# Optimization experiments

Measured on AMD Instinct MI355X. Metric: run time of the kernel, lower is better.

## Reference

```python
import jax, jax.numpy as jnp
import numpy as np

# Fixed hyperparameters matching init_kwargs
DIL_START = 2
DIL_END = 1024   # n_dilations = 1022
N_BULGE = 2
BATCH, L, C = 8, 2048, 4


def _variant_tables():
    """Static (forward_shift, backward_shift, has_GU) table, one row per output feature.
    Order per distance s: [main AU_CG+GU, left bulge d=1..n, right bulge d=1..n]."""
    f, b, g = [], [], []
    for s in range(DIL_START, DIL_END):
        f.append(s + 1); b.append(s + 1); g.append(1.0)            # dilate
        for d in range(1, N_BULGE + 1):                            # left bulge
            f.append(s + 1); b.append(s + 1 + d); g.append(0.0)
        for d in range(1, N_BULGE + 1):                            # right bulge
            f.append(s + 1 + d); b.append(s + 1); g.append(0.0)
    return np.array(f), np.array(b), np.array(g, dtype=np.float32)


def setup_inputs() -> dict:
    key = jax.random.key(0)
    x = jax.random.uniform(key, (BATCH, L, C), dtype=jnp.float32)
    return {"x": x}


def reference(x) -> jnp.ndarray:
    n, L_, _ = x.shape
    f_np, b_np, g_np = _variant_tables()
    f_arr = jnp.asarray(f_np)
    b_arr = jnp.asarray(b_np)
    gu_arr = jnp.asarray(g_np).astype(x.dtype)
    max_f = int(f_np.max())
    max_b = int(b_np.max())

    # y[i] = x[i+f] (zeros past the end);  z[i] = x[i-b] (zeros before start)
    xp_r = jnp.pad(x, ((0, 0), (0, max_f), (0, 0)))
    xp_l = jnp.pad(x, ((0, 0), (max_b, 0), (0, 0)))
    w4 = jnp.array([2.0, 3.0, 3.0, 2.0], dtype=x.dtype)  # AU/CG pairing weights

    def variant(f, b, g):
        y = jax.lax.dynamic_slice_in_dim(xp_r, f, L_, axis=1)          # (n, L, 4)
        z = jax.lax.dynamic_slice_in_dim(xp_l, max_b - b, L_, axis=1)  # (n, L, 4)
        # base: sum_c w[c] * x[i+f, c] * x[i-b, 3-c]  (reverse-complement correlation)
        base = jnp.einsum('nlc,nlc->nl', y * w4, z[..., ::-1])
        # GU wobble pairs (channels 2,3), weight 2, only for the non-bulge variant
        gu = 2.0 * (y[..., 2] * z[..., 3] + y[..., 3] * z[..., 2])
        return base + g * gu

    out = jax.vmap(variant)(f_arr, b_arr, gu_arr)  # (F, n, L)
    return jnp.transpose(out, (1, 2, 0))           # (n, L, F)
```

## Files before the change

### kernel.cpp

```cpp
#include <hip/hip_runtime.h>

#define LSEQ 2048
#define NS   1022
#define NF   5110
#define NB   8
#define IT   64
#define GI   4
#define NGRP (IT / GI)
#define TPB  256
#define FPB  (TPB * 5)

__device__ __forceinline__ float basescore(const float4 y, const float4 z) {
    return 2.f * y.x * z.w + 3.f * y.y * z.z + 3.f * y.z * z.y + 2.f * y.w * z.x;
}

__device__ __forceinline__ float4 loadx(const float4* __restrict__ xg, int p) {
    int pc = p < 0 ? 0 : (p > LSEQ - 1 ? LSEQ - 1 : p);
    float4 v = xg[pc];
    if ((unsigned)p >= (unsigned)LSEQ) v = make_float4(0.f, 0.f, 0.f, 0.f);
    return v;
}

__global__ __launch_bounds__(TPB) void fdcnn_kernel(const float4* __restrict__ x,
                                                    float* __restrict__ out) {
    __shared__ float st[2][GI][FPB];

    const int t = threadIdx.x;
    const int n = blockIdx.z;
    const float4* xg = x + (size_t)n * LSEQ;

    const int sidx = blockIdx.x * TPB + t;
    const int s = sidx + 2;
    const int i0 = blockIdx.y * IT;
    const int fbase = blockIdx.x * FPB;

    float4 yA = loadx(xg, i0 + s + 1);
    float4 yB = loadx(xg, i0 + s + 2);
    float4 zA = loadx(xg, i0 - s - 3);
    float4 zB = loadx(xg, i0 - s - 2);

    auto compute_group = [&](int g) {
        float* stg = &st[g & 1][0][0];
        #pragma unroll
        for (int ig = 0; ig < GI; ++ig) {
            const int i = i0 + g * GI + ig;
            float4 yC = loadx(xg, i + s + 3);
            float4 zC = loadx(xg, i - s - 1);
            const float4 y1 = yA, y2 = yB, y3 = yC;
            const float4 z3 = zA, z2 = zB, z1 = zC;
            float* sp = stg + ig * FPB + t * 5;
            sp[0] = basescore(y1, z1) + 2.f * (y1.z * z1.w + y1.w * z1.z);
            sp[1] = basescore(y1, z2);
            sp[2] = basescore(y1, z3);
            sp[3] = basescore(y2, z1);
            sp[4] = basescore(y3, z1);
            yA = yB; yB = yC;
            zA = zB; zB = zC;
        }
    };

    compute_group(0);

    for (int g = 0; g < NGRP; ++g) {
        asm volatile("s_waitcnt lgkmcnt(0)\n\ts_barrier" ::: "memory");

        if (g + 1 < NGRP) compute_group(g + 1);

        const float* stg = &st[g & 1][0][0];
        float* obase = out + ((size_t)n * LSEQ + (i0 + g * GI)) * (size_t)NF + fbase;
        #pragma unroll
        for (int k = 0; k < 5; ++k) {
            const int v  = k * TPB + t;
            const int ig = v / 320;
            const int fo = (v - ig * 320) * 4;
            const int rem = NF - (fbase + fo);
            const float4 val = *(const float4*)(stg + ig * FPB + fo);
            float* dst = obase + (size_t)ig * NF + fo;
            if (rem >= 4) {
                *(float4*)dst = val;
            } else if (rem > 0) {
                dst[0] = val.x;
                if (rem > 1) dst[1] = val.y;
            }
        }
    }
}

extern "C" void kernel_launch(void* const* d_in, const int* in_sizes, int n_in,
                              void* d_out, int out_size, void* d_ws, size_t ws_size,
                              hipStream_t stream) {
    const float4* x = (const float4*)d_in[0];
    float* out = (float*)d_out;
    dim3 grid((NS + TPB - 1) / TPB, LSEQ / IT, NB);
    dim3 block(TPB);
    fdcnn_kernel<<<grid, block, 0, stream>>>(x, out);
}
```

Baseline: 76.83 us.

## Interleave row groups across blocks and prefetch next group's inputs before stores

Each block now handles strided groups of 4 rows (stride 128 rows) instead of a contiguous 64-row tile, so concurrently running blocks write to rows spread across the output. The next group's inputs are loaded into registers before the current group's stores are issued, and the compute into shared memory happens after the stores, letting global loads overlap the write phase. Each group now reloads 6 float4 per sequence instead of sliding the window, and launch bounds ask for 4 blocks per CU. The output is a large store-bound tensor, so the gain depends on write locality and overlap.

```diff
diff --git a/kernel.cpp b/kernel.cpp
--- a/kernel.cpp
+++ b/kernel.cpp
@@ -4,9 +4,8 @@
 #define NS   1022
 #define NF   5110
 #define NB   8
-#define IT   64
 #define GI   4
-#define NGRP (IT / GI)
+#define NGRP 16
 #define TPB  256
 #define FPB  (TPB * 5)
 
@@ -21,53 +20,59 @@
     return v;
 }
 
-__global__ __launch_bounds__(TPB) void fdcnn_kernel(const float4* __restrict__ x,
-                                                    float* __restrict__ out) {
+__global__ __launch_bounds__(TPB, 4) void fdcnn_kernel(const float4* __restrict__ x,
+                                                       float* __restrict__ out) {
     __shared__ float st[2][GI][FPB];
 
     const int t = threadIdx.x;
+    const int bx = blockIdx.x;
+    const int by = blockIdx.y;
     const int n = blockIdx.z;
     const float4* xg = x + (size_t)n * LSEQ;
+    const int s = bx * TPB + t + 2;
+    const int fbase = bx * FPB;
 
-    const int sidx = blockIdx.x * TPB + t;
-    const int s = sidx + 2;
-    const int i0 = blockIdx.y * IT;
-    const int fbase = blockIdx.x * FPB;
-
-    float4 yA = loadx(xg, i0 + s + 1);
-    float4 yB = loadx(xg, i0 + s + 2);
-    float4 zA = loadx(xg, i0 - s - 3);
-    float4 zB = loadx(xg, i0 - s - 2);
-
-    auto compute_group = [&](int g) {
-        float* stg = &st[g & 1][0][0];
+    auto compute_to = [&](const float4* Y, const float4* Z, float* stg) {
         #pragma unroll
-        for (int ig = 0; ig < GI; ++ig) {
-            const int i = i0 + g * GI + ig;
-            float4 yC = loadx(xg, i + s + 3);
-            float4 zC = loadx(xg, i - s - 1);
-            const float4 y1 = yA, y2 = yB, y3 = yC;
-            const float4 z3 = zA, z2 = zB, z1 = zC;
-            float* sp = stg + ig * FPB + t * 5;
+        for (int ii = 0; ii < GI; ++ii) {
+            const float4 y1 = Y[ii], y2 = Y[ii + 1], y3 = Y[ii + 2];
+            const float4 z1 = Z[ii + 2], z2 = Z[ii + 1], z3 = Z[ii];
+            float* sp = stg + ii * FPB + t * 5;
             sp[0] = basescore(y1, z1) + 2.f * (y1.z * z1.w + y1.w * z1.z);
             sp[1] = basescore(y1, z2);
             sp[2] = basescore(y1, z3);
             sp[3] = basescore(y2, z1);
             sp[4] = basescore(y3, z1);
-            yA = yB; yB = yC;
-            zA = zB; zB = zC;
         }
     };
 
-    compute_group(0);
+    {
+        const int i0 = 4 * by;
+        float4 Y[6], Z[6];
+        #pragma unroll
+        for (int j = 0; j < 6; ++j) {
+            Y[j] = loadx(xg, i0 + s + 1 + j);
+            Z[j] = loadx(xg, i0 - s - 3 + j);
+        }
+        compute_to(Y, Z, &st[0][0][0]);
+    }
 
     for (int g = 0; g < NGRP; ++g) {
         asm volatile("s_waitcnt lgkmcnt(0)\n\ts_barrier" ::: "memory");
 
-        if (g + 1 < NGRP) compute_group(g + 1);
+        float4 Yn[6], Zn[6];
+        if (g + 1 < NGRP) {
+            const int i1 = 4 * (by + 32 * (g + 1));
+            #pragma unroll
+            for (int j = 0; j < 6; ++j) {
+                Yn[j] = loadx(xg, i1 + s + 1 + j);
+                Zn[j] = loadx(xg, i1 - s - 3 + j);
+            }
+        }
 
         const float* stg = &st[g & 1][0][0];
-        float* obase = out + ((size_t)n * LSEQ + (i0 + g * GI)) * (size_t)NF + fbase;
+        const int ig0 = 4 * (by + 32 * g);
+        float* obase = out + ((size_t)n * LSEQ + ig0) * (size_t)NF + fbase;
         #pragma unroll
         for (int k = 0; k < 5; ++k) {
             const int v  = k * TPB + t;
@@ -83,6 +88,8 @@
                 if (rem > 1) dst[1] = val.y;
             }
         }
+
+        if (g + 1 < NGRP) compute_to(Yn, Zn, &st[(g + 1) & 1][0][0]);
     }
 }
 
@@ -91,7 +98,7 @@
                               hipStream_t stream) {
     const float4* x = (const float4*)d_in[0];
     float* out = (float*)d_out;
-    dim3 grid((NS + TPB - 1) / TPB, LSEQ / IT, NB);
+    dim3 grid(4, 32, NB);
     dim3 block(TPB);
     fdcnn_kernel<<<grid, block, 0, stream>>>(x, out);
 }
```

New measurement: 73.43 us. -4.4%, faster.

## Stage input windows in per-wave LDS and drop block-wide barriers

Applied to the files above, without the earlier changes.

Each wave now loads its own sliding windows of x into shared memory once, instead of doing clamped global loads per row. The output staging buffer is also made per-wave, so the block-level s_barrier and the double buffering are removed. Each wave computes and stores its own strip of 320 features. The kernel is dominated by output writes, so the gain probably depends on whether removing barrier stalls lets stores stream more smoothly. The change also uses more LDS per block and sets a launch-bounds occupancy hint.

```diff
diff --git a/kernel.cpp b/kernel.cpp
--- a/kernel.cpp
+++ b/kernel.cpp
@@ -8,7 +8,9 @@
 #define GI   4
 #define NGRP (IT / GI)
 #define TPB  256
-#define FPB  (TPB * 5)
+#define NWAVE 4
+#define WSTRIP 320
+#define WLEN 132
 
 __device__ __forceinline__ float basescore(const float4 y, const float4 z) {
     return 2.f * y.x * z.w + 3.f * y.y * z.z + 3.f * y.z * z.y + 2.f * y.w * z.x;
@@ -21,34 +23,46 @@
     return v;
 }
 
-__global__ __launch_bounds__(TPB) void fdcnn_kernel(const float4* __restrict__ x,
-                                                    float* __restrict__ out) {
-    __shared__ float st[2][GI][FPB];
+__global__ __launch_bounds__(TPB, 4) void fdcnn_kernel(const float4* __restrict__ x,
+                                                       float* __restrict__ out) {
+    __shared__ float4 ysw[NWAVE][WLEN];
+    __shared__ float4 zsw[NWAVE][WLEN];
+    __shared__ float  stg[NWAVE][GI * WSTRIP];
 
     const int t = threadIdx.x;
+    const int w = t >> 6;
+    const int l = t & 63;
+    const int bx = blockIdx.x;
+    const int by = blockIdx.y;
     const int n = blockIdx.z;
+    const int i0 = by * IT;
     const float4* xg = x + (size_t)n * LSEQ;
 
-    const int sidx = blockIdx.x * TPB + t;
-    const int s = sidx + 2;
-    const int i0 = blockIdx.y * IT;
-    const int fbase = blockIdx.x * FPB;
+    const int s0 = bx * TPB + w * 64 + 2;
+    const int fwave = (bx * NWAVE + w) * WSTRIP;
 
-    float4 yA = loadx(xg, i0 + s + 1);
-    float4 yB = loadx(xg, i0 + s + 2);
-    float4 zA = loadx(xg, i0 - s - 3);
-    float4 zB = loadx(xg, i0 - s - 2);
+    const int base_y = i0 + s0 + 1;
+    const int base_z = i0 - s0 - 66;
+    #pragma unroll
+    for (int j = l; j < 129; j += 64) {
+        ysw[w][j] = loadx(xg, base_y + j);
+        zsw[w][j] = loadx(xg, base_z + j);
+    }
 
-    auto compute_group = [&](int g) {
-        float* stg = &st[g & 1][0][0];
+    float4 yA = ysw[w][l];
+    float4 yB = ysw[w][l + 1];
+    float4 zA = zsw[w][63 - l];
+    float4 zB = zsw[w][64 - l];
+
+    for (int g = 0; g < NGRP; ++g) {
         #pragma unroll
         for (int ig = 0; ig < GI; ++ig) {
-            const int i = i0 + g * GI + ig;
-            float4 yC = loadx(xg, i + s + 3);
-            float4 zC = loadx(xg, i - s - 1);
+            const int ii = g * GI + ig;
+            float4 yC = ysw[w][ii + l + 2];
+            float4 zC = zsw[w][ii + 65 - l];
             const float4 y1 = yA, y2 = yB, y3 = yC;
             const float4 z3 = zA, z2 = zB, z1 = zC;
-            float* sp = stg + ig * FPB + t * 5;
+            float* sp = &stg[w][ig * WSTRIP + l * 5];
             sp[0] = basescore(y1, z1) + 2.f * (y1.z * z1.w + y1.w * z1.z);
             sp[1] = basescore(y1, z2);
             sp[2] = basescore(y1, z3);
@@ -57,24 +71,16 @@
             yA = yB; yB = yC;
             zA = zB; zB = zC;
         }
-    };
 
-    compute_group(0);
-
-    for (int g = 0; g < NGRP; ++g) {
-        asm volatile("s_waitcnt lgkmcnt(0)\n\ts_barrier" ::: "memory");
-
-        if (g + 1 < NGRP) compute_group(g + 1);
-
-        const float* stg = &st[g & 1][0][0];
-        float* obase = out + ((size_t)n * LSEQ + (i0 + g * GI)) * (size_t)NF + fbase;
+        const int ibase = i0 + g * GI;
+        float* obase = out + ((size_t)n * LSEQ + ibase) * (size_t)NF + fwave;
         #pragma unroll
         for (int k = 0; k < 5; ++k) {
-            const int v  = k * TPB + t;
-            const int ig = v / 320;
-            const int fo = (v - ig * 320) * 4;
-            const int rem = NF - (fbase + fo);
-            const float4 val = *(const float4*)(stg + ig * FPB + fo);
+            const int v  = k * 64 + l;
+            const int ig = v / 80;
+            const int fo = (v - ig * 80) * 4;
+            const int rem = NF - (fwave + fo);
+            const float4 val = *(const float4*)&stg[w][ig * WSTRIP + fo];
             float* dst = obase + (size_t)ig * NF + fo;
             if (rem >= 4) {
                 *(float4*)dst = val;
@@ -91,7 +97,7 @@
                               hipStream_t stream) {
     const float4* x = (const float4*)d_in[0];
     float* out = (float*)d_out;
-    dim3 grid((NS + TPB - 1) / TPB, LSEQ / IT, NB);
+    dim3 grid(4, LSEQ / IT, NB);
     dim3 block(TPB);
     fdcnn_kernel<<<grid, block, 0, stream>>>(x, out);
 }
```

After: 77.73 us. Within noise of the previous version (+1.2%).
